# Kernel tuning notes

Hardware: AMD Instinct MI355X
Metric: run time of the kernel (lower is better)

Reference implementation:

```python
import math
import jax, jax.numpy as jnp
import numpy as np

B, S, H = 2, 2048, 2048
N_HEADS, N_KV_HEADS = 16, 4
HEAD_DIM = H // N_HEADS  # 128
ROPE_BASE = 10000.0


def setup_inputs() -> dict:
    key = jax.random.key(0)
    ks = jax.random.split(key, 8)
    hidden_states = jax.random.normal(ks[0], (B, S, H), dtype=jnp.float32)
    # continuous, increasing timestamps in [0, S)
    time_values = jnp.sort(jax.random.uniform(ks[1], (B, S), dtype=jnp.float32) * S, axis=-1)
    sc = 1.0 / math.sqrt(H)
    wq = jax.random.normal(ks[2], (H, N_HEADS * HEAD_DIM), dtype=jnp.float32) * sc
    bq = jnp.zeros((N_HEADS * HEAD_DIM,), dtype=jnp.float32)
    wk = jax.random.normal(ks[3], (H, N_KV_HEADS * HEAD_DIM), dtype=jnp.float32) * sc
    bk = jnp.zeros((N_KV_HEADS * HEAD_DIM,), dtype=jnp.float32)
    wv = jax.random.normal(ks[4], (H, N_KV_HEADS * HEAD_DIM), dtype=jnp.float32) * sc
    bv = jnp.zeros((N_KV_HEADS * HEAD_DIM,), dtype=jnp.float32)
    wo = jax.random.normal(ks[5], (N_HEADS * HEAD_DIM, H), dtype=jnp.float32) * sc
    # learnable per-dimension frequency modulation (init ones, as in module)
    rope_w = jnp.ones((HEAD_DIM // 2,), dtype=jnp.float32)
    return {"hidden_states": hidden_states, "time_values": time_values,
            "wq": wq, "bq": bq, "wk": wk, "bk": bk, "wv": wv, "bv": bv,
            "wo": wo, "rope_w": rope_w}


def _rotate_half(x):
    x1, x2 = jnp.split(x, 2, axis=-1)
    return jnp.concatenate((-x2, x1), axis=-1)


def reference(hidden_states, time_values, wq, bq, wk, bk, wv, bv, wo, rope_w):
    b, s, h = hidden_states.shape
    # QKV projections -> [b, heads, s, head_dim]
    q = (hidden_states @ wq + bq).reshape(b, s, N_HEADS, HEAD_DIM).transpose(0, 2, 1, 3)
    k = (hidden_states @ wk + bk).reshape(b, s, N_KV_HEADS, HEAD_DIM).transpose(0, 2, 1, 3)
    v = (hidden_states @ wv + bv).reshape(b, s, N_KV_HEADS, HEAD_DIM).transpose(0, 2, 1, 3)
    # Continuous-time RoPE: freqs = t * inv_freq * w  -> [b, s, hd/2]
    inv_freq = 1.0 / (ROPE_BASE ** (jnp.arange(0, HEAD_DIM, 2, dtype=jnp.float32) / HEAD_DIM))
    freqs = time_values[:, :, None] * inv_freq * rope_w
    emb = jnp.concatenate((freqs, freqs), axis=-1)[:, None]  # [b, 1, s, hd]
    cos = jnp.cos(emb).astype(q.dtype)
    sin = jnp.sin(emb).astype(q.dtype)
    q = q * cos + _rotate_half(q) * sin
    k = k * cos + _rotate_half(k) * sin
    # GQA: repeat_kv
    n_rep = N_HEADS // N_KV_HEADS
    k = jnp.repeat(k, n_rep, axis=1)
    v = jnp.repeat(v, n_rep, axis=1)
    # scaled dot-product attention, causal
    scale = 1.0 / math.sqrt(HEAD_DIM)
    scores = jnp.einsum('bhqd,bhkd->bhqk', q, k) * scale
    causal = jnp.tril(jnp.ones((s, s), dtype=bool))
    scores = jnp.where(causal, scores, jnp.finfo(scores.dtype).min)
    attn = jax.nn.softmax(scores, axis=-1)
    out = jnp.einsum('bhqk,bhkd->bhqd', attn, v)  # [b, nh, s, hd]
    out = out.transpose(0, 2, 1, 3).reshape(b, s, N_HEADS * HEAD_DIM)
    return out @ wo
```

## Files before the change

kernel.cpp:

```cpp
#include <hip/hip_runtime.h>


#define S_LEN 2048
#define BATCH 2
#define NH    16
#define NKV   4
#define HD    128

typedef float  f32x4  __attribute__((ext_vector_type(4)));
typedef __bf16 bf16x8 __attribute__((ext_vector_type(8)));
typedef __bf16 bf16x4 __attribute__((ext_vector_type(4)));
typedef unsigned int u32x4 __attribute__((ext_vector_type(4)));
typedef unsigned int u32x2 __attribute__((ext_vector_type(2)));

__device__ inline unsigned short f2bf(float f) {
    unsigned u = __builtin_bit_cast(unsigned, f);
    unsigned r = (u + 0x7fffu + ((u >> 16) & 1u)) >> 16;
    return (unsigned short)r;
}

__device__ inline void gload_lds16(const void* g, void* l) {
    __builtin_amdgcn_global_load_lds(
        (const __attribute__((address_space(1))) unsigned int*)g,
        (__attribute__((address_space(3))) unsigned int*)l, 16, 0, 0);
}

__global__ void transpose_qkv(const float* __restrict__ wq,
                              const float* __restrict__ wk,
                              const float* __restrict__ wv,
                              unsigned short* __restrict__ Wt) {
    int z = blockIdx.z;
    const float* src = (z == 0) ? wq : ((z == 1) ? wk : wv);
    int C = (z == 0) ? 2048 : 512;
    long doff = (z == 0) ? 0L : ((z == 1) ? 2048L * 2048 : 2560L * 2048);
    int bx = blockIdx.x * 32, by = blockIdx.y * 32;
    if (bx >= C) return;
    __shared__ unsigned short t[32][33];
    int x = threadIdx.x, y0 = threadIdx.y;
    #pragma unroll
    for (int i = 0; i < 4; i++) {
        int y = y0 + i * 8;
        t[y][x] = f2bf(src[(long)(by + y) * C + bx + x]);
    }
    __syncthreads();
    #pragma unroll
    for (int i = 0; i < 4; i++) {
        int y = y0 + i * 8;
        Wt[doff + (long)(bx + y) * 2048 + by + x] = t[x][y];
    }
}

__global__ void transpose_to_bf16(const float* __restrict__ src,
                                  unsigned short* __restrict__ dst,
                                  int R, int C, long dst_off, int ldd) {
    __shared__ unsigned short t[32][33];
    int bx = blockIdx.x * 32, by = blockIdx.y * 32;
    int x = threadIdx.x, y0 = threadIdx.y;
    #pragma unroll
    for (int i = 0; i < 4; i++) {
        int y = y0 + i * 8;
        t[y][x] = f2bf(src[(long)(by + y) * C + bx + x]);
    }
    __syncthreads();
    #pragma unroll
    for (int i = 0; i < 4; i++) {
        int y = y0 + i * 8;
        dst[dst_off + (long)(bx + y) * ldd + by + x] = t[x][y];
    }
}

__global__ __launch_bounds__(256) void prep_kernel(
        const float* __restrict__ X, unsigned short* __restrict__ Xb,
        const float* __restrict__ bq, const float* __restrict__ bk,
        const float* __restrict__ bv, float* __restrict__ bsf,
        const float* __restrict__ tv, const float* __restrict__ rw,
        unsigned int* __restrict__ Tab) {
    int bi = blockIdx.x, tid = threadIdx.x;
    long i = ((long)bi * 256 + tid) * 8;
    {
        f32x4 a = *(const f32x4*)&X[i];
        f32x4 b = *(const f32x4*)&X[i + 4];
        u32x4 r;
        r.x = (unsigned)f2bf(a[0]) | ((unsigned)f2bf(a[1]) << 16);
        r.y = (unsigned)f2bf(a[2]) | ((unsigned)f2bf(a[3]) << 16);
        r.z = (unsigned)f2bf(b[0]) | ((unsigned)f2bf(b[1]) << 16);
        r.w = (unsigned)f2bf(b[2]) | ((unsigned)f2bf(b[3]) << 16);
        *(u32x4*)&Xb[i] = r;
    }
    if (bi < 12) {
        int ib = bi * 256 + tid;
        bsf[ib] = (ib < 2048) ? bq[ib] : ((ib < 2560) ? bk[ib - 2048] : bv[ib - 2560]);
    }
    if (bi < 1024) {
        int m = bi * 4 + (tid >> 6);
        int fi = tid & 63;
        float t = tv[m];
        float f = t * powf(10000.f, -(float)fi / 64.f) * rw[fi];
        Tab[m * 64 + fi] = (unsigned)f2bf(cosf(f)) | ((unsigned)f2bf(sinf(f)) << 16);
    }
}

__device__ __forceinline__ void stage_half(const unsigned short* __restrict__ G,
        int baseRow, long kc, unsigned short* slot, int r0, int c0, int tid) {
    gload_lds16(&G[(long)(baseRow + r0) * 2048 + kc + c0], &slot[tid * 8]);
    gload_lds16(&G[(long)(baseRow + r0 + 128) * 2048 + kc + c0], &slot[4096 + tid * 8]);
}

#define STG_A(buf, ks, kt) \
    stage_half(A,  m0, (long)(kt) * 64 + (ks) * 32, &sm[(buf) * 16384 + (ks) * 8192], r0s, c0s, tid)
#define STG_B(buf, ks, kt) \
    stage_half(Bt, n0, (long)(kt) * 64 + (ks) * 32, &sm[32768 + (buf) * 16384 + (ks) * 8192], r0s, c0s, tid)

#define NOPV ((void)0)
#define VM6  asm volatile("s_waitcnt vmcnt(6)" ::: "memory")

#define PH(buf, ks, mh, RDB, STG, VM)                                          \
    {                                                                          \
        const int sb_ = (buf) * 16384 + (ks) * 8192;                           \
        bf16x8 a0 = *(const bf16x8*)&sm[sb_ + abase + (mh) * 2048];            \
        bf16x8 a1 = *(const bf16x8*)&sm[sb_ + abase + (mh) * 2048 + 512];      \
        bf16x8 a2 = *(const bf16x8*)&sm[sb_ + abase + (mh) * 2048 + 1024];     \
        bf16x8 a3 = *(const bf16x8*)&sm[sb_ + abase + (mh) * 2048 + 1536];     \
        if (RDB) {                                                             \
            b0 = *(const bf16x8*)&sm[sb_ + bbase];                             \
            b1 = *(const bf16x8*)&sm[sb_ + bbase + 512];                       \
            b2 = *(const bf16x8*)&sm[sb_ + bbase + 1024];                      \
            b3 = *(const bf16x8*)&sm[sb_ + bbase + 1536];                      \
        }                                                                      \
        STG;                                                                   \
        VM;                                                                    \
        __builtin_amdgcn_s_barrier();                                          \
        asm volatile("s_waitcnt lgkmcnt(0)" ::: "memory");                     \
        __builtin_amdgcn_sched_barrier(0);                                     \
        __builtin_amdgcn_s_setprio(1);                                         \
        _Pragma("unroll") for (int mi = 0; mi < 4; ++mi) {                     \
            bf16x8 am = (mi == 0) ? a0 : (mi == 1) ? a1 : (mi == 2) ? a2 : a3; \
            acc[(mh) * 4 + mi][0] = __builtin_amdgcn_mfma_f32_16x16x32_bf16(   \
                am, b0, acc[(mh) * 4 + mi][0], 0, 0, 0);                       \
            acc[(mh) * 4 + mi][1] = __builtin_amdgcn_mfma_f32_16x16x32_bf16(   \
                am, b1, acc[(mh) * 4 + mi][1], 0, 0, 0);                       \
            acc[(mh) * 4 + mi][2] = __builtin_amdgcn_mfma_f32_16x16x32_bf16(   \
                am, b2, acc[(mh) * 4 + mi][2], 0, 0, 0);                       \
            acc[(mh) * 4 + mi][3] = __builtin_amdgcn_mfma_f32_16x16x32_bf16(   \
                am, b3, acc[(mh) * 4 + mi][3], 0, 0, 0);                       \
        }                                                                      \
        __builtin_amdgcn_s_setprio(0);                                         \
        __builtin_amdgcn_s_barrier();                                          \
    }

__global__ __launch_bounds__(512, 2) void gemm_qkv_rope(
        const unsigned short* __restrict__ A,
        const unsigned short* __restrict__ Bt,
        const float* __restrict__ bsf,
        const unsigned int* __restrict__ Tab,
        unsigned short* __restrict__ Qr,
        unsigned short* __restrict__ Kr,
        unsigned short* __restrict__ Vt) {
    __shared__ __align__(16) unsigned short sm[65536];

    const int tid = threadIdx.x;
    const int wid = tid >> 6, lane = tid & 63, quad = lane >> 4, l16 = lane & 15;
    const int wr = wid >> 2, wc = wid & 3;

    const int u   = blockIdx.y * 12 + blockIdx.x;
    const int swz = (u & 7) * 24 + (u >> 3);
    const int bx  = swz % 12;
    const int m0  = (swz / 12) * 256;
    const int n0  = bx * 256;

    const int sg    = (quad ^ ((l16 >> 1) & 3)) * 8;
    const int abase = wr * 4096 + l16 * 32 + sg;
    const int bbase = 32768 + wc * 2048 + l16 * 32 + sg;

    const int r0s = tid >> 2;
    const int c0s = ((tid & 3) ^ ((r0s >> 1) & 3)) * 8;

    f32x4 acc[8][4];
    #pragma unroll
    for (int i = 0; i < 8; i++)
        #pragma unroll
        for (int j = 0; j < 4; j++)
            #pragma unroll
            for (int c = 0; c < 4; c++) acc[i][j][c] = 0.f;
    bf16x8 b0 = {}, b1 = {}, b2 = {}, b3 = {};

    STG_B(0, 0, 0); STG_A(0, 0, 0); STG_B(0, 1, 0); STG_A(0, 1, 0);
    STG_B(1, 0, 1); STG_A(1, 0, 1); STG_B(1, 1, 1);
    asm volatile("s_waitcnt vmcnt(6)" ::: "memory");
    __builtin_amdgcn_s_barrier();

    for (int it = 0; it < 16; ++it) {
        const int t1  = 2 * it + 1;
        const int tn0 = (it < 15) ? 2 * it + 2 : 31;
        const int tn1 = (it < 15) ? 2 * it + 3 : 31;
        PH(0, 0, 0, 1, STG_A(1, 1, t1),  NOPV);
        PH(0, 0, 1, 0, STG_B(0, 0, tn0), NOPV);
        PH(0, 1, 0, 1, STG_A(0, 0, tn0), NOPV);
        PH(0, 1, 1, 0, STG_B(0, 1, tn0), VM6);
        PH(1, 0, 0, 1, STG_A(0, 1, tn0), NOPV);
        PH(1, 0, 1, 0, STG_B(1, 0, tn1), NOPV);
        PH(1, 1, 0, 1, STG_A(1, 0, tn1), NOPV);
        PH(1, 1, 1, 0, STG_B(1, 1, tn1), VM6);
    }

    asm volatile("s_waitcnt vmcnt(0)" ::: "memory");
    __syncthreads();

    float* Ep = (float*)sm;
    const int EPLD = 264;
    float bv4[4];
    #pragma unroll
    for (int ni = 0; ni < 4; ++ni) bv4[ni] = bsf[n0 + wc * 64 + ni * 16 + l16];
    const bool isV = (bx >= 10);
    const float qs = (bx < 8) ? (0.08838834764831845f * 1.4426950408889634f) : 1.0f;

    const int lt = tid >> 4, hh = (tid >> 3) & 1, jj = tid & 7, j0 = jj * 8;
    const int vd = tid >> 1, vsh = tid & 1;

    #pragma unroll
    for (int p = 0; p < 8; ++p) {
        if (wr == (p >> 2)) {
            #pragma unroll
            for (int f = 0; f < 2; ++f) {
                #pragma unroll
                for (int ni = 0; ni < 4; ++ni)
                    #pragma unroll
                    for (int r = 0; r < 4; ++r)
                        Ep[(f * 16 + quad * 4 + r) * EPLD + wc * 64 + ni * 16 + l16] =
                            acc[(p & 3) * 2 + f][ni][r] + bv4[ni];
            }
        }
        __syncthreads();
        if (!isV) {
            const int gm = m0 + p * 32 + lt;
            const int bb = gm >> 11, s = gm & 2047;
            unsigned short* dst = (bx < 8)
                ? Qr + ((long)(bb * NH + bx * 2 + hh) * S_LEN + s) * HD
                : Kr + ((long)(bb * NKV + (bx - 8) * 2 + hh) * S_LEN + s) * HD;
            u32x4 t0 = *(const u32x4*)&Tab[(long)gm * 64 + j0];
            u32x4 t1v = *(const u32x4*)&Tab[(long)gm * 64 + j0 + 4];
            f32x4 x1a = *(f32x4*)&Ep[lt * EPLD + hh * 128 + j0];
            f32x4 x1b = *(f32x4*)&Ep[lt * EPLD + hh * 128 + j0 + 4];
            f32x4 x2a = *(f32x4*)&Ep[lt * EPLD + hh * 128 + 64 + j0];
            f32x4 x2b = *(f32x4*)&Ep[lt * EPLD + hh * 128 + 64 + j0 + 4];
            f32x4 la, lb, ha, hb;
            #pragma unroll
            for (int e = 0; e < 4; e++) {
                float ca = __builtin_bit_cast(float, t0[e] << 16);
                float sa = __builtin_bit_cast(float, t0[e] & 0xffff0000u);
                float cb = __builtin_bit_cast(float, t1v[e] << 16);
                float sbv = __builtin_bit_cast(float, t1v[e] & 0xffff0000u);
                la[e] = (x1a[e] * ca - x2a[e] * sa) * qs;
                ha[e] = (x2a[e] * ca + x1a[e] * sa) * qs;
                lb[e] = (x1b[e] * cb - x2b[e] * sbv) * qs;
                hb[e] = (x2b[e] * cb + x1b[e] * sbv) * qs;
            }
            u32x4 lo, hi;
            lo.x = (unsigned)f2bf(la[0]) | ((unsigned)f2bf(la[1]) << 16);
            lo.y = (unsigned)f2bf(la[2]) | ((unsigned)f2bf(la[3]) << 16);
            lo.z = (unsigned)f2bf(lb[0]) | ((unsigned)f2bf(lb[1]) << 16);
            lo.w = (unsigned)f2bf(lb[2]) | ((unsigned)f2bf(lb[3]) << 16);
            hi.x = (unsigned)f2bf(ha[0]) | ((unsigned)f2bf(ha[1]) << 16);
            hi.y = (unsigned)f2bf(ha[2]) | ((unsigned)f2bf(ha[3]) << 16);
            hi.z = (unsigned)f2bf(hb[0]) | ((unsigned)f2bf(hb[1]) << 16);
            hi.w = (unsigned)f2bf(hb[2]) | ((unsigned)f2bf(hb[3]) << 16);
            *(u32x4*)&dst[j0] = lo;
            *(u32x4*)&dst[64 + j0] = hi;
        } else {
            const int gmb = m0 + p * 32 + vsh * 16;
            const int bb = gmb >> 11, s0 = gmb & 2047;
            const int vh = (bx - 10) * 2 + (vd >> 7), dl = vd & 127;
            unsigned short* dst = Vt + ((long)(bb * NKV + vh) * HD + dl) * S_LEN + s0;
            unsigned short pv[16];
            #pragma unroll
            for (int t = 0; t < 16; ++t)
                pv[t] = f2bf(Ep[(vsh * 16 + t) * EPLD + vd]);
            u32x4 v0, v1;
            v0.x = (unsigned)pv[0]  | ((unsigned)pv[1]  << 16);
            v0.y = (unsigned)pv[2]  | ((unsigned)pv[3]  << 16);
            v0.z = (unsigned)pv[4]  | ((unsigned)pv[5]  << 16);
            v0.w = (unsigned)pv[6]  | ((unsigned)pv[7]  << 16);
            v1.x = (unsigned)pv[8]  | ((unsigned)pv[9]  << 16);
            v1.y = (unsigned)pv[10] | ((unsigned)pv[11] << 16);
            v1.z = (unsigned)pv[12] | ((unsigned)pv[13] << 16);
            v1.w = (unsigned)pv[14] | ((unsigned)pv[15] << 16);
            *(u32x4*)&dst[0] = v0;
            *(u32x4*)&dst[8] = v1;
        }
        __syncthreads();
    }
}

template <typename CT>
__global__ __launch_bounds__(256) void gemm_bt_async(
        const unsigned short* __restrict__ A,
        const unsigned short* __restrict__ Bt,
        CT* __restrict__ C,
        const float* __restrict__ bias,
        int K, int lda, int ldb, int ldc) {
    __shared__ __align__(16) unsigned short As[128 * 64];
    __shared__ __align__(16) unsigned short Bs[128 * 64];
    const int tid = threadIdx.x;
    const int wid = tid >> 6, lane = tid & 63, quad = lane >> 4, l16 = lane & 15;
    const int wr = wid >> 1, wc = wid & 1;
    const int m0 = blockIdx.y * 128, n0 = blockIdx.x * 128;
    const int l7 = l16 & 7;

    f32x4 acc[4][4];
    #pragma unroll
    for (int i = 0; i < 4; i++)
        #pragma unroll
        for (int j = 0; j < 4; j++)
            #pragma unroll
            for (int c = 0; c < 4; c++) acc[i][j][c] = 0.f;

    for (int k0 = 0; k0 < K; k0 += 64) {
        #pragma unroll
        for (int i = 0; i < 4; i++) {
            int c = tid + 256 * i;
            int row = c >> 3, loct = ((c & 7) ^ (row & 7)) * 8;
            gload_lds16(&A[(long)(m0 + row) * lda + k0 + loct], &As[c * 8]);
        }
        #pragma unroll
        for (int i = 0; i < 4; i++) {
            int c = tid + 256 * i;
            int row = c >> 3, loct = ((c & 7) ^ (row & 7)) * 8;
            gload_lds16(&Bt[(long)(n0 + row) * ldb + k0 + loct], &Bs[c * 8]);
        }
        __syncthreads();
        #pragma unroll
        for (int s = 0; s < 2; s++) {
            bf16x8 af[4], bfr[4];
            #pragma unroll
            for (int mi = 0; mi < 4; mi++)
                af[mi] = *(const bf16x8*)
                    &As[(wr * 64 + mi * 16 + l16) * 64 + (((s * 4 + quad) ^ l7)) * 8];
            #pragma unroll
            for (int ni = 0; ni < 4; ni++)
                bfr[ni] = *(const bf16x8*)
                    &Bs[(wc * 64 + ni * 16 + l16) * 64 + (((s * 4 + quad) ^ l7)) * 8];
            #pragma unroll
            for (int mi = 0; mi < 4; mi++)
                #pragma unroll
                for (int ni = 0; ni < 4; ni++)
                    acc[mi][ni] = __builtin_amdgcn_mfma_f32_16x16x32_bf16(
                        af[mi], bfr[ni], acc[mi][ni], 0, 0, 0);
        }
        __syncthreads();
    }

    #pragma unroll
    for (int mi = 0; mi < 4; mi++) {
        #pragma unroll
        for (int ni = 0; ni < 4; ni++) {
            int gn = n0 + wc * 64 + ni * 16 + l16;
            float bv_ = bias ? bias[gn] : 0.f;
            #pragma unroll
            for (int r = 0; r < 4; r++) {
                int gm = m0 + wr * 64 + mi * 16 + quad * 4 + r;
                float v = acc[mi][ni][r] + bv_;
                if constexpr (sizeof(CT) == 4) C[(long)gm * ldc + gn] = v;
                else                           C[(long)gm * ldc + gn] = f2bf(v);
            }
        }
    }
}

__global__ __launch_bounds__(512, 4) void attn_kernel(
        const unsigned short* __restrict__ Qr,
        const unsigned short* __restrict__ Kr,
        const unsigned short* __restrict__ Vt,
        unsigned short* __restrict__ Out) {
    __shared__ __align__(16) unsigned short Ks[64 * 128];
    __shared__ __align__(16) unsigned short Vs[128 * 64];
    __shared__ __align__(16) unsigned short Ps[8][16 * 68];

    const int h = blockIdx.x, b = blockIdx.z;
    const int qt = b ? blockIdx.y : (int)(gridDim.y - 1 - blockIdx.y);
    const int tid = threadIdx.x, w = tid >> 6, lane = tid & 63;
    const int quad = lane >> 4, l16 = lane & 15;
    const int hk = h >> 2;
    const unsigned short* Qb = Qr + (long)((b * NH + h) * S_LEN) * HD;
    const unsigned short* Kb = Kr + (long)((b * NKV + hk) * S_LEN) * HD;
    const unsigned short* Vb = Vt + (long)((b * NKV + hk) * HD) * S_LEN;
    const int qw = qt * 128 + w * 16;
    const int q  = qw + l16;
    const float MASK_MIN = -3.0e38f;

    bf16x8 qf[4];
    #pragma unroll
    for (int kc = 0; kc < 4; kc++)
        qf[kc] = *(const bf16x8*)&Qb[(long)q * HD + kc * 32 + quad * 8];

    f32x4 o[8];
    #pragma unroll
    for (int db = 0; db < 8; db++)
        #pragma unroll
        for (int c = 0; c < 4; c++) o[db][c] = 0.f;
    float mr = MASK_MIN, lr = 0.f;

    const int sK0 = tid, sK1 = tid + 512;
    const int kR0 = sK0 >> 4, kC0 = ((sK0 & 15) ^ (kR0 & 15)) * 8;
    const int kR1 = sK1 >> 4, kC1 = ((sK1 & 15) ^ (kR1 & 15)) * 8;
    const int vR0 = sK0 >> 3, vC0 = ((sK0 & 7) ^ (vR0 & 7)) * 8;
    const int vR1 = sK1 >> 3, vC1 = ((sK1 & 7) ^ (vR1 & 7)) * 8;

    const int nkt = 2 * qt + 2;
    for (int kt = 0; kt < nkt; kt++) {
        const int k0 = kt * 64;
        __syncthreads();
        gload_lds16(&Kb[(long)(k0 + kR0) * HD + kC0], &Ks[sK0 * 8]);
        gload_lds16(&Kb[(long)(k0 + kR1) * HD + kC1], &Ks[sK1 * 8]);
        gload_lds16(&Vb[(long)vR0 * S_LEN + k0 + vC0], &Vs[sK0 * 8]);
        gload_lds16(&Vb[(long)vR1 * S_LEN + k0 + vC1], &Vs[sK1 * 8]);
        __syncthreads();

        if (k0 > qw + 15) continue;

        f32x4 sc[4];
        #pragma unroll
        for (int nb = 0; nb < 4; nb++) {
            #pragma unroll
            for (int c = 0; c < 4; c++) sc[nb][c] = 0.f;
            #pragma unroll
            for (int kc = 0; kc < 4; kc++) {
                bf16x8 kf = *(const bf16x8*)
                    &Ks[(nb * 16 + l16) * 128 + (((kc * 4 + quad) ^ l16) * 8)];
                sc[nb] = __builtin_amdgcn_mfma_f32_16x16x32_bf16(kf, qf[kc], sc[nb], 0, 0, 0);
            }
        }
        if (k0 + 63 > qw) {
            #pragma unroll
            for (int nb = 0; nb < 4; nb++) {
                int kvb = k0 + nb * 16 + quad * 4;
                #pragma unroll
                for (int r = 0; r < 4; r++)
                    sc[nb][r] = (kvb + r > q) ? MASK_MIN : sc[nb][r];
            }
        }
        float tm = MASK_MIN;
        #pragma unroll
        for (int nb = 0; nb < 4; nb++)
            #pragma unroll
            for (int r = 0; r < 4; r++) tm = fmaxf(tm, sc[nb][r]);
        tm = fmaxf(tm, __shfl_xor(tm, 16));
        tm = fmaxf(tm, __shfl_xor(tm, 32));

        float mn = mr;
        if (__any(tm > mr)) {
            mn = fmaxf(mr, tm);
            float alpha = exp2f(mr - mn);
            mr = mn;
            lr *= alpha;
            #pragma unroll
            for (int db = 0; db < 8; db++)
                #pragma unroll
                for (int c = 0; c < 4; c++) o[db][c] *= alpha;
        }
        float rs = 0.f;
        #pragma unroll
        for (int nb = 0; nb < 4; nb++) {
            float pv0 = exp2f(sc[nb][0] - mn), pv1 = exp2f(sc[nb][1] - mn);
            float pv2 = exp2f(sc[nb][2] - mn), pv3 = exp2f(sc[nb][3] - mn);
            rs += (pv0 + pv1) + (pv2 + pv3);
            bf16x4 pk4 = { (__bf16)pv0, (__bf16)pv1, (__bf16)pv2, (__bf16)pv3 };
            *(bf16x4*)&Ps[w][l16 * 68 + nb * 16 + quad * 4] = pk4;
        }
        rs += __shfl_xor(rs, 16);
        rs += __shfl_xor(rs, 32);
        lr += rs;

        #pragma unroll
        for (int kk = 0; kk < 2; kk++) {
            bf16x8 pf = *(const bf16x8*)&Ps[w][l16 * 68 + kk * 32 + quad * 8];
            #pragma unroll
            for (int db = 0; db < 8; db++) {
                bf16x8 vf = *(const bf16x8*)
                    &Vs[(db * 16 + l16) * 64 + (((kk * 4 + quad) ^ (l16 & 7)) * 8)];
                o[db] = __builtin_amdgcn_mfma_f32_16x16x32_bf16(vf, pf, o[db], 0, 0, 0);
            }
        }
    }

    float inv_l = 1.0f / lr;
    long obase = (long)(b * S_LEN + q) * 2048 + h * 128 + quad * 4;
    #pragma unroll
    for (int db = 0; db < 8; db++) {
        bf16x4 pk4 = { (__bf16)(o[db][0] * inv_l), (__bf16)(o[db][1] * inv_l),
                       (__bf16)(o[db][2] * inv_l), (__bf16)(o[db][3] * inv_l) };
        *(bf16x4*)&Out[obase + db * 16] = pk4;
    }
}

extern "C" void kernel_launch(void* const* d_in, const int* in_sizes, int n_in,
                              void* d_out, int out_size, void* d_ws, size_t ws_size,
                              hipStream_t stream) {
    const float* X  = (const float*)d_in[0];
    const float* tv = (const float*)d_in[1];
    const float* wq = (const float*)d_in[2];
    const float* bq = (const float*)d_in[3];
    const float* wk = (const float*)d_in[4];
    const float* bk = (const float*)d_in[5];
    const float* wv = (const float*)d_in[6];
    const float* bv = (const float*)d_in[7];
    const float* wo = (const float*)d_in[8];
    const float* rw = (const float*)d_in[9];

    char* ws = (char*)d_ws;
    unsigned short* Wt  = (unsigned short*)ws; ws += 3072L * 2048 * 2;
    float*          bsf = (float*)ws;          ws += 3072L * 4;
    unsigned int*   Tab = (unsigned int*)ws;   ws += 4096L * 64 * 4;
    unsigned short* Qr  = (unsigned short*)ws; ws += (long)BATCH * NH  * S_LEN * HD * 2;
    unsigned short* Kr  = (unsigned short*)ws; ws += (long)BATCH * NKV * S_LEN * HD * 2;
    unsigned short* Vt  = (unsigned short*)ws; ws += (long)BATCH * NKV * HD * S_LEN * 2;
    unsigned short* AO  = (unsigned short*)ws; ws += 4096L * 2048 * 2;
    unsigned short* Xb  = AO;

    transpose_qkv<<<dim3(64, 64, 3), dim3(32, 8), 0, stream>>>(wq, wk, wv, Wt);
    prep_kernel<<<4096, 256, 0, stream>>>(X, Xb, bq, bk, bv, bsf, tv, rw, Tab);
    gemm_qkv_rope<<<dim3(12, 16), 512, 0, stream>>>(Xb, Wt, bsf, Tab, Qr, Kr, Vt);
    transpose_to_bf16<<<dim3(64, 64), dim3(32, 8), 0, stream>>>(wo, Wt, 2048, 2048, 0L, 2048);
    attn_kernel<<<dim3(NH, S_LEN / 128, BATCH), 512, 0, stream>>>(Qr, Kr, Vt, AO);
    gemm_bt_async<float><<<dim3(16, 32), 256, 0, stream>>>(
        AO, Wt, (float*)d_out, nullptr, 2048, 2048, 2048, 2048);
}
```

Baseline: 303.1 us.

## Pair causal query tiles per attention block and reuse pipelined GEMM for output projection

The attention kernel now assigns each block two query tiles (qt and 15-qt), so every block does the same amount of causal work and the paired tiles share each K/V tile load. K/V tiles are double-buffered in LDS with the next tile prefetched during compute. The output projection moves from a simple 128x128 GEMM to the 256x256 software-pipelined GEMM body already used for QKV, factored into a shared macro. The cost is more registers and LDS per attention block and fewer blocks in the grid (256 attention, 128 GEMM), which may leave parts of the device underused.

```diff
diff --git a/kernel.cpp b/kernel.cpp
--- a/kernel.cpp
+++ b/kernel.cpp
@@ -148,6 +148,25 @@
         __builtin_amdgcn_s_barrier();                                          \
     }
 
+#define GEMM_PRO_LOOP(NIT)                                                     \
+    STG_B(0, 0, 0); STG_A(0, 0, 0); STG_B(0, 1, 0); STG_A(0, 1, 0);            \
+    STG_B(1, 0, 1); STG_A(1, 0, 1); STG_B(1, 1, 1);                            \
+    asm volatile("s_waitcnt vmcnt(6)" ::: "memory");                           \
+    __builtin_amdgcn_s_barrier();                                              \
+    for (int it = 0; it < (NIT); ++it) {                                       \
+        const int t1  = 2 * it + 1;                                            \
+        const int tn0 = (it < (NIT) - 1) ? 2 * it + 2 : 2 * (NIT) - 1;         \
+        const int tn1 = (it < (NIT) - 1) ? 2 * it + 3 : 2 * (NIT) - 1;         \
+        PH(0, 0, 0, 1, STG_A(1, 1, t1),  NOPV);                                \
+        PH(0, 0, 1, 0, STG_B(0, 0, tn0), NOPV);                                \
+        PH(0, 1, 0, 1, STG_A(0, 0, tn0), NOPV);                                \
+        PH(0, 1, 1, 0, STG_B(0, 1, tn0), VM6);                                 \
+        PH(1, 0, 0, 1, STG_A(0, 1, tn0), NOPV);                                \
+        PH(1, 0, 1, 0, STG_B(1, 0, tn1), NOPV);                                \
+        PH(1, 1, 0, 1, STG_A(1, 0, tn1), NOPV);                                \
+        PH(1, 1, 1, 0, STG_B(1, 1, tn1), VM6);                                 \
+    }
+
 __global__ __launch_bounds__(512, 2) void gemm_qkv_rope(
         const unsigned short* __restrict__ A,
         const unsigned short* __restrict__ Bt,
@@ -184,24 +203,7 @@
             for (int c = 0; c < 4; c++) acc[i][j][c] = 0.f;
     bf16x8 b0 = {}, b1 = {}, b2 = {}, b3 = {};
 
-    STG_B(0, 0, 0); STG_A(0, 0, 0); STG_B(0, 1, 0); STG_A(0, 1, 0);
-    STG_B(1, 0, 1); STG_A(1, 0, 1); STG_B(1, 1, 1);
-    asm volatile("s_waitcnt vmcnt(6)" ::: "memory");
-    __builtin_amdgcn_s_barrier();
-
-    for (int it = 0; it < 16; ++it) {
-        const int t1  = 2 * it + 1;
-        const int tn0 = (it < 15) ? 2 * it + 2 : 31;
-        const int tn1 = (it < 15) ? 2 * it + 3 : 31;
-        PH(0, 0, 0, 1, STG_A(1, 1, t1),  NOPV);
-        PH(0, 0, 1, 0, STG_B(0, 0, tn0), NOPV);
-        PH(0, 1, 0, 1, STG_A(0, 0, tn0), NOPV);
-        PH(0, 1, 1, 0, STG_B(0, 1, tn0), VM6);
-        PH(1, 0, 0, 1, STG_A(0, 1, tn0), NOPV);
-        PH(1, 0, 1, 0, STG_B(1, 0, tn1), NOPV);
-        PH(1, 1, 0, 1, STG_A(1, 0, tn1), NOPV);
-        PH(1, 1, 1, 0, STG_B(1, 1, tn1), VM6);
-    }
+    GEMM_PRO_LOOP(16)
 
     asm volatile("s_waitcnt vmcnt(0)" ::: "memory");
     __syncthreads();
@@ -291,113 +293,168 @@
     }
 }
 
-template <typename CT>
-__global__ __launch_bounds__(256) void gemm_bt_async(
+__global__ __launch_bounds__(512, 2) void gemm_o(
         const unsigned short* __restrict__ A,
         const unsigned short* __restrict__ Bt,
-        CT* __restrict__ C,
-        const float* __restrict__ bias,
-        int K, int lda, int ldb, int ldc) {
-    __shared__ __align__(16) unsigned short As[128 * 64];
-    __shared__ __align__(16) unsigned short Bs[128 * 64];
+        float* __restrict__ C) {
+    __shared__ __align__(16) unsigned short sm[65536];
+
     const int tid = threadIdx.x;
     const int wid = tid >> 6, lane = tid & 63, quad = lane >> 4, l16 = lane & 15;
-    const int wr = wid >> 1, wc = wid & 1;
-    const int m0 = blockIdx.y * 128, n0 = blockIdx.x * 128;
-    const int l7 = l16 & 7;
-
-    f32x4 acc[4][4];
-    #pragma unroll
-    for (int i = 0; i < 4; i++)
+    const int wr = wid >> 2, wc = wid & 3;
+
+    const int u   = blockIdx.y * 8 + blockIdx.x;
+    const int swz = (u & 7) * 16 + (u >> 3);
+    const int m0  = (swz >> 3) * 256;
+    const int n0  = (swz & 7) * 256;
+
+    const int sg    = (quad ^ ((l16 >> 1) & 3)) * 8;
+    const int abase = wr * 4096 + l16 * 32 + sg;
+    const int bbase = 32768 + wc * 2048 + l16 * 32 + sg;
+    const int r0s = tid >> 2;
+    const int c0s = ((tid & 3) ^ ((r0s >> 1) & 3)) * 8;
+
+    f32x4 acc[8][4];
+    #pragma unroll
+    for (int i = 0; i < 8; i++)
         #pragma unroll
         for (int j = 0; j < 4; j++)
             #pragma unroll
             for (int c = 0; c < 4; c++) acc[i][j][c] = 0.f;
-
-    for (int k0 = 0; k0 < K; k0 += 64) {
-        #pragma unroll
-        for (int i = 0; i < 4; i++) {
-            int c = tid + 256 * i;
-            int row = c >> 3, loct = ((c & 7) ^ (row & 7)) * 8;
-            gload_lds16(&A[(long)(m0 + row) * lda + k0 + loct], &As[c * 8]);
-        }
-        #pragma unroll
-        for (int i = 0; i < 4; i++) {
-            int c = tid + 256 * i;
-            int row = c >> 3, loct = ((c & 7) ^ (row & 7)) * 8;
-            gload_lds16(&Bt[(long)(n0 + row) * ldb + k0 + loct], &Bs[c * 8]);
-        }
-        __syncthreads();
-        #pragma unroll
-        for (int s = 0; s < 2; s++) {
-            bf16x8 af[4], bfr[4];
-            #pragma unroll
-            for (int mi = 0; mi < 4; mi++)
-                af[mi] = *(const bf16x8*)
-                    &As[(wr * 64 + mi * 16 + l16) * 64 + (((s * 4 + quad) ^ l7)) * 8];
-            #pragma unroll
-            for (int ni = 0; ni < 4; ni++)
-                bfr[ni] = *(const bf16x8*)
-                    &Bs[(wc * 64 + ni * 16 + l16) * 64 + (((s * 4 + quad) ^ l7)) * 8];
-            #pragma unroll
-            for (int mi = 0; mi < 4; mi++)
-                #pragma unroll
-                for (int ni = 0; ni < 4; ni++)
-                    acc[mi][ni] = __builtin_amdgcn_mfma_f32_16x16x32_bf16(
-                        af[mi], bfr[ni], acc[mi][ni], 0, 0, 0);
-        }
-        __syncthreads();
-    }
-
-    #pragma unroll
-    for (int mi = 0; mi < 4; mi++) {
-        #pragma unroll
-        for (int ni = 0; ni < 4; ni++) {
-            int gn = n0 + wc * 64 + ni * 16 + l16;
-            float bv_ = bias ? bias[gn] : 0.f;
-            #pragma unroll
-            for (int r = 0; r < 4; r++) {
-                int gm = m0 + wr * 64 + mi * 16 + quad * 4 + r;
-                float v = acc[mi][ni][r] + bv_;
-                if constexpr (sizeof(CT) == 4) C[(long)gm * ldc + gn] = v;
-                else                           C[(long)gm * ldc + gn] = f2bf(v);
+    bf16x8 b0 = {}, b1 = {}, b2 = {}, b3 = {};
+
+    GEMM_PRO_LOOP(16)
+
+    asm volatile("s_waitcnt vmcnt(0)" ::: "memory");
+
+    #pragma unroll
+    for (int j = 0; j < 8; ++j)
+        #pragma unroll
+        for (int ni = 0; ni < 4; ++ni) {
+            const int gn = n0 + wc * 64 + ni * 16 + l16;
+            #pragma unroll
+            for (int r = 0; r < 4; ++r) {
+                const int gm = m0 + wr * 128 + (j >> 2) * 64 + (j & 3) * 16 + quad * 4 + r;
+                C[(long)gm * 2048 + gn] = acc[j][ni][r];
             }
         }
-    }
-}
-
-__global__ __launch_bounds__(512, 4) void attn_kernel(
+}
+
+__device__ __forceinline__ void attn_chunk(
+        const unsigned short* __restrict__ Ksb,
+        const unsigned short* __restrict__ Vsb,
+        unsigned short* __restrict__ Psw,
+        const bf16x8* __restrict__ qf,
+        f32x4* __restrict__ o, float& mr, float& lr,
+        int k0, int qw, int q, int quad, int l16) {
+    const float MASK_MIN = -3.0e38f;
+    f32x4 sc[4];
+    #pragma unroll
+    for (int nb = 0; nb < 4; nb++)
+        #pragma unroll
+        for (int c = 0; c < 4; c++) sc[nb][c] = 0.f;
+
+    __builtin_amdgcn_s_setprio(1);
+    #pragma unroll
+    for (int nb = 0; nb < 4; nb++)
+        #pragma unroll
+        for (int kc = 0; kc < 4; kc++) {
+            bf16x8 kf = *(const bf16x8*)
+                &Ksb[(nb * 16 + l16) * 128 + (((kc * 4 + quad) ^ l16) * 8)];
+            sc[nb] = __builtin_amdgcn_mfma_f32_16x16x32_bf16(kf, qf[kc], sc[nb], 0, 0, 0);
+        }
+    __builtin_amdgcn_s_setprio(0);
+
+    if (k0 + 63 > qw) {
+        #pragma unroll
+        for (int nb = 0; nb < 4; nb++) {
+            int kvb = k0 + nb * 16 + quad * 4;
+            #pragma unroll
+            for (int r = 0; r < 4; r++)
+                sc[nb][r] = (kvb + r > q) ? MASK_MIN : sc[nb][r];
+        }
+    }
+    float tm = MASK_MIN;
+    #pragma unroll
+    for (int nb = 0; nb < 4; nb++)
+        #pragma unroll
+        for (int r = 0; r < 4; r++) tm = fmaxf(tm, sc[nb][r]);
+    tm = fmaxf(tm, __shfl_xor(tm, 16));
+    tm = fmaxf(tm, __shfl_xor(tm, 32));
+
+    float mn = mr;
+    if (__any(tm > mr)) {
+        mn = fmaxf(mr, tm);
+        float alpha = exp2f(mr - mn);
+        mr = mn;
+        lr *= alpha;
+        #pragma unroll
+        for (int db = 0; db < 8; db++)
+            #pragma unroll
+            for (int c = 0; c < 4; c++) o[db][c] *= alpha;
+    }
+    float rs = 0.f;
+    #pragma unroll
+    for (int nb = 0; nb < 4; nb++) {
+        float pv0 = exp2f(sc[nb][0] - mn), pv1 = exp2f(sc[nb][1] - mn);
+        float pv2 = exp2f(sc[nb][2] - mn), pv3 = exp2f(sc[nb][3] - mn);
+        rs += (pv0 + pv1) + (pv2 + pv3);
+        bf16x4 pk4 = { (__bf16)pv0, (__bf16)pv1, (__bf16)pv2, (__bf16)pv3 };
+        *(bf16x4*)&Psw[l16 * 68 + nb * 16 + quad * 4] = pk4;
+    }
+    rs += __shfl_xor(rs, 16);
+    rs += __shfl_xor(rs, 32);
+    lr += rs;
+
+    __builtin_amdgcn_s_setprio(1);
+    #pragma unroll
+    for (int kk = 0; kk < 2; kk++) {
+        bf16x8 pf = *(const bf16x8*)&Psw[l16 * 68 + kk * 32 + quad * 8];
+        #pragma unroll
+        for (int db = 0; db < 8; db++) {
+            bf16x8 vf = *(const bf16x8*)
+                &Vsb[(db * 16 + l16) * 64 + (((kk * 4 + quad) ^ (l16 & 7)) * 8)];
+            o[db] = __builtin_amdgcn_mfma_f32_16x16x32_bf16(vf, pf, o[db], 0, 0, 0);
+        }
+    }
+    __builtin_amdgcn_s_setprio(0);
+}
+
+__global__ __launch_bounds__(512, 2) void attn_kernel(
         const unsigned short* __restrict__ Qr,
         const unsigned short* __restrict__ Kr,
         const unsigned short* __restrict__ Vt,
         unsigned short* __restrict__ Out) {
-    __shared__ __align__(16) unsigned short Ks[64 * 128];
-    __shared__ __align__(16) unsigned short Vs[128 * 64];
+    __shared__ __align__(16) unsigned short Ks[2][64 * 128];
+    __shared__ __align__(16) unsigned short Vs[2][128 * 64];
     __shared__ __align__(16) unsigned short Ps[8][16 * 68];
 
     const int h = blockIdx.x, b = blockIdx.z;
-    const int qt = b ? blockIdx.y : (int)(gridDim.y - 1 - blockIdx.y);
+    const int qtA = blockIdx.y;
+    const int qtB = 15 - qtA;
     const int tid = threadIdx.x, w = tid >> 6, lane = tid & 63;
     const int quad = lane >> 4, l16 = lane & 15;
     const int hk = h >> 2;
     const unsigned short* Qb = Qr + (long)((b * NH + h) * S_LEN) * HD;
     const unsigned short* Kb = Kr + (long)((b * NKV + hk) * S_LEN) * HD;
     const unsigned short* Vb = Vt + (long)((b * NKV + hk) * HD) * S_LEN;
-    const int qw = qt * 128 + w * 16;
-    const int q  = qw + l16;
+    const int qwA = qtA * 128 + w * 16, qA = qwA + l16;
+    const int qwB = qtB * 128 + w * 16, qB = qwB + l16;
     const float MASK_MIN = -3.0e38f;
 
-    bf16x8 qf[4];
-    #pragma unroll
-    for (int kc = 0; kc < 4; kc++)
-        qf[kc] = *(const bf16x8*)&Qb[(long)q * HD + kc * 32 + quad * 8];
-
-    f32x4 o[8];
+    bf16x8 qfA[4], qfB[4];
+    #pragma unroll
+    for (int kc = 0; kc < 4; kc++) {
+        qfA[kc] = *(const bf16x8*)&Qb[(long)qA * HD + kc * 32 + quad * 8];
+        qfB[kc] = *(const bf16x8*)&Qb[(long)qB * HD + kc * 32 + quad * 8];
+    }
+
+    f32x4 oA[8], oB[8];
     #pragma unroll
     for (int db = 0; db < 8; db++)
         #pragma unroll
-        for (int c = 0; c < 4; c++) o[db][c] = 0.f;
-    float mr = MASK_MIN, lr = 0.f;
+        for (int c = 0; c < 4; c++) { oA[db][c] = 0.f; oB[db][c] = 0.f; }
+    float mrA = MASK_MIN, lrA = 0.f, mrB = MASK_MIN, lrB = 0.f;
 
     const int sK0 = tid, sK1 = tid + 512;
     const int kR0 = sK0 >> 4, kC0 = ((sK0 & 15) ^ (kR0 & 15)) * 8;
@@ -405,90 +462,51 @@
     const int vR0 = sK0 >> 3, vC0 = ((sK0 & 7) ^ (vR0 & 7)) * 8;
     const int vR1 = sK1 >> 3, vC1 = ((sK1 & 7) ^ (vR1 & 7)) * 8;
 
-    const int nkt = 2 * qt + 2;
-    for (int kt = 0; kt < nkt; kt++) {
+    const int nktB = 2 * qtB + 2;
+
+    gload_lds16(&Kb[(long)kR0 * HD + kC0], &Ks[0][sK0 * 8]);
+    gload_lds16(&Kb[(long)kR1 * HD + kC1], &Ks[0][sK1 * 8]);
+    gload_lds16(&Vb[(long)vR0 * S_LEN + vC0], &Vs[0][sK0 * 8]);
+    gload_lds16(&Vb[(long)vR1 * S_LEN + vC1], &Vs[0][sK1 * 8]);
+    __syncthreads();
+
+    int cur = 0;
+    for (int kt = 0; kt < nktB; kt++) {
         const int k0 = kt * 64;
+        if (kt + 1 < nktB) {
+            const int kn = k0 + 64;
+            gload_lds16(&Kb[(long)(kn + kR0) * HD + kC0], &Ks[cur ^ 1][sK0 * 8]);
+            gload_lds16(&Kb[(long)(kn + kR1) * HD + kC1], &Ks[cur ^ 1][sK1 * 8]);
+            gload_lds16(&Vb[(long)vR0 * S_LEN + kn + vC0], &Vs[cur ^ 1][sK0 * 8]);
+            gload_lds16(&Vb[(long)vR1 * S_LEN + kn + vC1], &Vs[cur ^ 1][sK1 * 8]);
+        }
+        if (k0 <= qwA + 15)
+            attn_chunk(Ks[cur], Vs[cur], Ps[w], qfA, oA, mrA, lrA, k0, qwA, qA, quad, l16);
+        if (k0 <= qwB + 15)
+            attn_chunk(Ks[cur], Vs[cur], Ps[w], qfB, oB, mrB, lrB, k0, qwB, qB, quad, l16);
         __syncthreads();
-        gload_lds16(&Kb[(long)(k0 + kR0) * HD + kC0], &Ks[sK0 * 8]);
-        gload_lds16(&Kb[(long)(k0 + kR1) * HD + kC1], &Ks[sK1 * 8]);
-        gload_lds16(&Vb[(long)vR0 * S_LEN + k0 + vC0], &Vs[sK0 * 8]);
-        gload_lds16(&Vb[(long)vR1 * S_LEN + k0 + vC1], &Vs[sK1 * 8]);
-        __syncthreads();
-
-        if (k0 > qw + 15) continue;
-
-        f32x4 sc[4];
-        #pragma unroll
-        for (int nb = 0; nb < 4; nb++) {
-            #pragma unroll
-            for (int c = 0; c < 4; c++) sc[nb][c] = 0.f;
-            #pragma unroll
-            for (int kc = 0; kc < 4; kc++) {
-                bf16x8 kf = *(const bf16x8*)
-                    &Ks[(nb * 16 + l16) * 128 + (((kc * 4 + quad) ^ l16) * 8)];
-                sc[nb] = __builtin_amdgcn_mfma_f32_16x16x32_bf16(kf, qf[kc], sc[nb], 0, 0, 0);
-            }
-        }
-        if (k0 + 63 > qw) {
-            #pragma unroll
-            for (int nb = 0; nb < 4; nb++) {
-                int kvb = k0 + nb * 16 + quad * 4;
-                #pragma unroll
-                for (int r = 0; r < 4; r++)
-                    sc[nb][r] = (kvb + r > q) ? MASK_MIN : sc[nb][r];
-            }
-        }
-        float tm = MASK_MIN;
-        #pragma unroll
-        for (int nb = 0; nb < 4; nb++)
-            #pragma unroll
-            for (int r = 0; r < 4; r++) tm = fmaxf(tm, sc[nb][r]);
-        tm = fmaxf(tm, __shfl_xor(tm, 16));
-        tm = fmaxf(tm, __shfl_xor(tm, 32));
-
-        float mn = mr;
-        if (__any(tm > mr)) {
-            mn = fmaxf(mr, tm);
-            float alpha = exp2f(mr - mn);
-            mr = mn;
-            lr *= alpha;
-            #pragma unroll
-            for (int db = 0; db < 8; db++)
-                #pragma unroll
-                for (int c = 0; c < 4; c++) o[db][c] *= alpha;
-        }
-        float rs = 0.f;
-        #pragma unroll
-        for (int nb = 0; nb < 4; nb++) {
-            float pv0 = exp2f(sc[nb][0] - mn), pv1 = exp2f(sc[nb][1] - mn);
-            float pv2 = exp2f(sc[nb][2] - mn), pv3 = exp2f(sc[nb][3] - mn);
-            rs += (pv0 + pv1) + (pv2 + pv3);
-            bf16x4 pk4 = { (__bf16)pv0, (__bf16)pv1, (__bf16)pv2, (__bf16)pv3 };
-            *(bf16x4*)&Ps[w][l16 * 68 + nb * 16 + quad * 4] = pk4;
-        }
-        rs += __shfl_xor(rs, 16);
-        rs += __shfl_xor(rs, 32);
-        lr += rs;
-
-        #pragma unroll
-        for (int kk = 0; kk < 2; kk++) {
-            bf16x8 pf = *(const bf16x8*)&Ps[w][l16 * 68 + kk * 32 + quad * 8];
-            #pragma unroll
-            for (int db = 0; db < 8; db++) {
-                bf16x8 vf = *(const bf16x8*)
-                    &Vs[(db * 16 + l16) * 64 + (((kk * 4 + quad) ^ (l16 & 7)) * 8)];
-                o[db] = __builtin_amdgcn_mfma_f32_16x16x32_bf16(vf, pf, o[db], 0, 0, 0);
-            }
-        }
-    }
-
-    float inv_l = 1.0f / lr;
-    long obase = (long)(b * S_LEN + q) * 2048 + h * 128 + quad * 4;
-    #pragma unroll
-    for (int db = 0; db < 8; db++) {
-        bf16x4 pk4 = { (__bf16)(o[db][0] * inv_l), (__bf16)(o[db][1] * inv_l),
-                       (__bf16)(o[db][2] * inv_l), (__bf16)(o[db][3] * inv_l) };
-        *(bf16x4*)&Out[obase + db * 16] = pk4;
+        cur ^= 1;
+    }
+
+    {
+        float inv_l = 1.0f / lrA;
+        long obase = (long)(b * S_LEN + qA) * 2048 + h * 128 + quad * 4;
+        #pragma unroll
+        for (int db = 0; db < 8; db++) {
+            bf16x4 pk4 = { (__bf16)(oA[db][0] * inv_l), (__bf16)(oA[db][1] * inv_l),
+                           (__bf16)(oA[db][2] * inv_l), (__bf16)(oA[db][3] * inv_l) };
+            *(bf16x4*)&Out[obase + db * 16] = pk4;
+        }
+    }
+    {
+        float inv_l = 1.0f / lrB;
+        long obase = (long)(b * S_LEN + qB) * 2048 + h * 128 + quad * 4;
+        #pragma unroll
+        for (int db = 0; db < 8; db++) {
+            bf16x4 pk4 = { (__bf16)(oB[db][0] * inv_l), (__bf16)(oB[db][1] * inv_l),
+                           (__bf16)(oB[db][2] * inv_l), (__bf16)(oB[db][3] * inv_l) };
+            *(bf16x4*)&Out[obase + db * 16] = pk4;
+        }
     }
 }
 
@@ -520,7 +538,6 @@
     prep_kernel<<<4096, 256, 0, stream>>>(X, Xb, bq, bk, bv, bsf, tv, rw, Tab);
     gemm_qkv_rope<<<dim3(12, 16), 512, 0, stream>>>(Xb, Wt, bsf, Tab, Qr, Kr, Vt);
     transpose_to_bf16<<<dim3(64, 64), dim3(32, 8), 0, stream>>>(wo, Wt, 2048, 2048, 0L, 2048);
-    attn_kernel<<<dim3(NH, S_LEN / 128, BATCH), 512, 0, stream>>>(Qr, Kr, Vt, AO);
-    gemm_bt_async<float><<<dim3(16, 32), 256, 0, stream>>>(
-        AO, Wt, (float*)d_out, nullptr, 2048, 2048, 2048, 2048);
-}
+    attn_kernel<<<dim3(NH, 8, BATCH), 512, 0, stream>>>(Qr, Kr, Vt, AO);
+    gemm_o<<<dim3(8, 16), 512, 0, stream>>>(AO, Wt, (float*)d_out);
+}
```

Result: slower. 320.6 us (+5.8%).
